# Kernel tuning notes

Hardware: AMD Instinct MI355X
Metric: run time of the kernel (lower is better)

## Reference

```python
import jax, jax.numpy as jnp
import numpy as np

B, N, D, DEPTH = 1, 512, 128, 4


def mlp_apply(W, x):
    # W: (depth, d, d), x: (..., d). First layer has no activation, then silu before each matmul.
    x = x @ W[0]
    for i in range(1, DEPTH):
        x = jax.nn.silu(x) @ W[i]
    return x


def _binop(x, y):
    # linear recurrence combine: s_t = a_t * s_{t-1} + b_t
    a1, b1 = x
    a2, b2 = y
    return (a1 * a2, a2 * b1 + b2)


def setup_inputs() -> dict:
    key = jax.random.key(0)
    ks = jax.random.split(key, 7)
    s = 0.02  # scale for projection weights (torch Linear-like init magnitude)
    return {
        "seq": jax.random.normal(ks[0], (B, N, D), jnp.float32),
        "W_mem": jax.random.normal(ks[1], (DEPTH, D, D), jnp.float32) * (D ** -0.5),
        "W_q": jax.random.normal(ks[2], (D, D), jnp.float32) * s,
        "W_kv": jax.random.normal(ks[3], (D, 2 * D), jnp.float32) * s,
        "W_mom": jax.random.normal(ks[4], (D, 1), jnp.float32) * s,
        "W_step": jax.random.normal(ks[5], (D, 1), jnp.float32) * s,
        "W_decay": jax.random.normal(ks[6], (D, 1), jnp.float32) * s,
    }


def reference(seq, W_mem, W_q, W_kv, W_mom, W_step, W_decay):
    b, n, d = seq.shape
    # --- store_memories ---
    adaptive_lr = (seq @ W_step)[..., 0]            # (b, n)
    adaptive_mom = seq @ W_mom                      # (b, n, 1)
    decay = jax.nn.sigmoid(seq @ W_decay)           # (b, n, 1)

    kv = seq.reshape(b * n, d) @ W_kv               # (bn, 2d)
    keys, values = kv[:, :d], kv[:, d:]

    def loss_fn(W, k, v):
        pred = mlp_apply(W, k)                      # (d,)
        # (pred - v)^2 .mean(-1).sum() for a single sample == mean over d
        return jnp.mean((pred - v) ** 2)

    # per-sample meta-gradients wrt memory MLP weights
    losses, grads = jax.vmap(jax.value_and_grad(loss_fn, argnums=0), in_axes=(None, 0, 0))(W_mem, keys, values)
    grads = grads.reshape(b, n, DEPTH, d, d)
    surprise = grads * (-adaptive_lr)[..., None, None, None]   # (b,n,depth,d,d)

    # momentum_t = adaptive_mom_t * momentum_{t-1} + surprise_t  (assoc. scan over n)
    am = adaptive_mom[..., None, None]              # (b, n, 1, 1, 1)
    _, momentum = jax.lax.associative_scan(_binop, (am, surprise), axis=1)

    # update_t = (1 - decay_t) * update_{t-1} + momentum_t
    dec = (1.0 - decay)[..., None, None]            # (b, n, 1, 1, 1)
    _, updates = jax.lax.associative_scan(_binop, (dec, momentum), axis=1)

    # --- retrieve_memories with per-token updated weights ---
    q = (seq @ W_q).reshape(b * n, d)
    W_tok = (W_mem[None, None] + updates).reshape(b * n, DEPTH, d, d)
    retrieved = jax.vmap(mlp_apply)(W_tok, q).reshape(b, n, d)
    return retrieved
```

## Files before the change

kernel.cpp:

```cpp
#include <hip/hip_runtime.h>
#include <hip/hip_bf16.h>
#include <math.h>

#define N 512
#define D 128
#define DD (D*D)
#define ND (N*D)
#define LSTR 132
#define CSTR 36

__device__ __forceinline__ float sigmoidf_(float x) { return 1.f / (1.f + expf(-x)); }

__global__ void k_transpose(const float* __restrict__ W_mem, float* __restrict__ WT) {
    int idx = blockIdx.x * 256 + threadIdx.x;
    int l = idx / DD;
    int r = idx % DD;
    int i = r / D;
    int j = r % D;
    WT[idx] = W_mem[(l + 1) * DD + j * D + i];
}

__global__ __launch_bounds__(512) void k_phase1(
    const float* __restrict__ seq, const float* __restrict__ W_mem,
    const float* __restrict__ W_q, const float* __restrict__ W_kv,
    const float* __restrict__ W_mom, const float* __restrict__ W_step,
    const float* __restrict__ W_decay, const float* __restrict__ WT,
    float* __restrict__ Q, float* __restrict__ INS, float* __restrict__ ES,
    float* __restrict__ am, float* __restrict__ dec)
{
    __shared__ float s_seq[D], s_v[D], s_cur[D];
    __shared__ float s_h[4][D];
    __shared__ float s_part[4][D];
    __shared__ float s_p3[4][3][D];
    __shared__ float s_red[8];
    __shared__ float s_lr;

    const int t = blockIdx.x;
    const int tid = threadIdx.x;
    const int j = tid & 127;
    const int p = tid >> 7;
    const int i0 = p * 32;

    if (p == 0) s_seq[j] = seq[t * D + j];
    __syncthreads();

    float ps = 0.f;
    if (p == 1) ps = s_seq[j] * W_step[j];
    else if (p == 2) ps = s_seq[j] * W_mom[j];
    else if (p == 3) ps = s_seq[j] * W_decay[j];
#pragma unroll
    for (int off = 32; off > 0; off >>= 1) ps += __shfl_down(ps, off);
    if ((tid & 63) == 0) s_red[tid >> 6] = ps;
    __syncthreads();
    if (tid == 0) s_lr = s_red[2] + s_red[3];
    else if (tid == 1) am[t] = s_red[4] + s_red[5];
    else if (tid == 2) dec[t] = 1.f - sigmoidf_(s_red[6] + s_red[7]);

    float kp = 0.f, vp = 0.f, qp = 0.f;
#pragma unroll 8
    for (int ii = 0; ii < 32; ii++) {
        int i = i0 + ii;
        float si = s_seq[i];
        kp += si * W_kv[i * 256 + j];
        vp += si * W_kv[i * 256 + 128 + j];
        qp += si * W_q[i * 128 + j];
    }
    s_p3[p][0][j] = kp; s_p3[p][1][j] = vp; s_p3[p][2][j] = qp;
    __syncthreads();
    if (p == 0) {
        float kj = s_p3[0][0][j] + s_p3[1][0][j] + s_p3[2][0][j] + s_p3[3][0][j];
        s_cur[j] = kj;
        INS[t * D + j] = kj;
    } else if (p == 1) {
        s_v[j] = s_p3[0][1][j] + s_p3[1][1][j] + s_p3[2][1][j] + s_p3[3][1][j];
    } else if (p == 2) {
        Q[t * D + j] = s_p3[0][2][j] + s_p3[1][2][j] + s_p3[2][2][j] + s_p3[3][2][j];
    }
    __syncthreads();

    for (int l = 0; l < 4; l++) {
        const float* Wl = W_mem + l * DD;
        float yp = 0.f;
#pragma unroll 8
        for (int ii = 0; ii < 32; ii++) {
            int i = i0 + ii;
            yp += s_cur[i] * Wl[i * D + j];
        }
        s_part[p][j] = yp;
        __syncthreads();
        if (p == 0) {
            float y = s_part[0][j] + s_part[1][j] + s_part[2][j] + s_part[3][j];
            s_h[l][j] = y;
            if (l < 3) {
                float a = y * sigmoidf_(y);
                s_cur[j] = a;
                INS[(l + 1) * ND + t * D + j] = a;
            }
        }
        __syncthreads();
    }

    if (p == 0) {
        float e = -s_lr * (2.f / (float)D) * (s_h[3][j] - s_v[j]);
        ES[3 * ND + t * D + j] = e;
        s_cur[j] = e;
    }
    __syncthreads();

    for (int l = 3; l >= 1; l--) {
        const float* Wt = WT + (l - 1) * DD;
        float gp = 0.f;
#pragma unroll 8
        for (int ii = 0; ii < 32; ii++) {
            int i = i0 + ii;
            gp += s_cur[i] * Wt[i * D + j];
        }
        s_part[p][j] = gp;
        __syncthreads();
        if (p == 0) {
            float g = s_part[0][j] + s_part[1][j] + s_part[2][j] + s_part[3][j];
            float h = s_h[l - 1][j];
            float sg = sigmoidf_(h);
            float e2 = g * (sg * (1.f + h * (1.f - sg)));
            ES[(l - 1) * ND + t * D + j] = e2;
            s_cur[j] = e2;
        }
        __syncthreads();
    }
}

__global__ __launch_bounds__(512) void k_logscan(
    const float* __restrict__ am, const float* __restrict__ dec,
    double* __restrict__ LA, double* __restrict__ LDp, int* __restrict__ NC)
{
    __shared__ double sa[N], sd[N];
    __shared__ int sn[N];
    const int t = threadIdx.x;
    float a = am[t];
    float d = dec[t];
    sa[t] = log((double)fmaxf(fabsf(a), 1e-38f));
    sd[t] = log((double)fmaxf(d, 1e-38f));
    sn[t] = (a < 0.f) ? 1 : 0;
    __syncthreads();
    for (int off = 1; off < N; off <<= 1) {
        double va = 0.0, vd = 0.0; int vn = 0;
        if (t >= off) { va = sa[t - off]; vd = sd[t - off]; vn = sn[t - off]; }
        __syncthreads();
        sa[t] += va; sd[t] += vd; sn[t] += vn;
        __syncthreads();
    }
    LA[t] = sa[t]; LDp[t] = sd[t]; NC[t] = sn[t];
}

__global__ __launch_bounds__(256) void k_build(
    const double* __restrict__ LA, const double* __restrict__ LDp,
    const int* __restrict__ NC,
    float* __restrict__ Amat, float* __restrict__ Dmat)
{
    int idx = blockIdx.x * 256 + threadIdx.x;
    int u = idx >> 9;
    int s = idx & (N - 1);
    float va = 0.f, vd = 0.f;
    if (s <= u) {
        va = expf((float)(LA[u] - LA[s]));
        if ((NC[u] - NC[s]) & 1) va = -va;
        vd = expf((float)(LDp[u] - LDp[s]));
    }
    Amat[idx] = va;
    Dmat[idx] = vd;
}

__global__ __launch_bounds__(256) void k_betamm(
    const float* __restrict__ Dmat, const float* __restrict__ Amat,
    float* __restrict__ beta)
{
    const int bs = blockIdx.x;
    const int bt = blockIdx.y;
    const int tx = threadIdx.x & 31;
    const int ty = threadIdx.x >> 5;

    if (bs > bt) {
#pragma unroll
        for (int j = 0; j < 4; j++)
            beta[(bt * 32 + ty + 8 * j) * N + bs * 32 + tx] = 0.f;
        return;
    }

    __shared__ float sD[32][33];
    __shared__ float sA[32][33];
    float acc[4] = {0.f, 0.f, 0.f, 0.f};

    for (int kt = bs; kt <= bt; kt++) {
        for (int i = threadIdx.x; i < 1024; i += 256) {
            int r = i >> 5, c = i & 31;
            sD[r][c] = Dmat[(bt * 32 + r) * N + kt * 32 + c];
            sA[r][c] = Amat[(kt * 32 + r) * N + bs * 32 + c];
        }
        __syncthreads();
#pragma unroll 8
        for (int k = 0; k < 32; k++) {
            float a = sA[k][tx];
#pragma unroll
            for (int j = 0; j < 4; j++)
                acc[j] += sD[ty + 8 * j][k] * a;
        }
        __syncthreads();
    }
#pragma unroll
    for (int j = 0; j < 4; j++)
        beta[(bt * 32 + ty + 8 * j) * N + bs * 32 + tx] = acc[j];
}

__global__ __launch_bounds__(256) void k_layer(
    const float* __restrict__ Xsrc, float* __restrict__ Pout,
    const float* __restrict__ Wl, const float* __restrict__ INSl,
    const float* __restrict__ ESl, const float* __restrict__ beta,
    int mode)
{
    const int r = blockIdx.x;
    const int z = blockIdx.y;
    const bool isW = (z == 8);
    if (!isW && 4 * z > r) return;
    const int t0 = r * 16;
    const int lane = threadIdx.x;

    __shared__ float sX[16 * LSTR];
    __shared__ float sI[32 * LSTR];
    __shared__ float sE[32 * LSTR];
    __shared__ float sc[16 * CSTR];

    const int nzs = (r >> 2) + 1;
#pragma unroll
    for (int i = 0; i < 2; i++) {
        int f4 = lane + 256 * i;
        int row = f4 >> 5, c4 = f4 & 31;
        float4 v = ((const float4*)(Xsrc + t0 * D))[f4];
        if (mode) {
            for (int zz = 1; zz < nzs; zz++) {
                float4 u = ((const float4*)(Xsrc + zz * ND + t0 * D))[f4];
                v.x += u.x; v.y += u.y; v.z += u.z; v.w += u.w;
            }
            float4 w = ((const float4*)(Xsrc + 8 * ND + t0 * D))[f4];
            v.x += w.x; v.y += w.y; v.z += w.z; v.w += w.w;
            v.x = v.x * sigmoidf_(v.x); v.y = v.y * sigmoidf_(v.y);
            v.z = v.z * sigmoidf_(v.z); v.w = v.w * sigmoidf_(v.w);
        }
        *(float4*)(sX + row * LSTR + c4 * 4) = v;
    }

    const int ti  = lane >> 4;
    const int q15 = lane & 15;
    const int j8  = q15 * 8;

    if (isW) {
        __syncthreads();
        float acc[8];
#pragma unroll
        for (int b = 0; b < 8; b++) acc[b] = 0.f;
#pragma unroll 4
        for (int k = 0; k < D; k++) {
            float4 w0 = *(const float4*)(Wl + k * D + j8);
            float4 w1 = *(const float4*)(Wl + k * D + j8 + 4);
            float xv = sX[ti * LSTR + k];
            acc[0] += xv * w0.x; acc[1] += xv * w0.y;
            acc[2] += xv * w0.z; acc[3] += xv * w0.w;
            acc[4] += xv * w1.x; acc[5] += xv * w1.y;
            acc[6] += xv * w1.z; acc[7] += xv * w1.w;
        }
        float* yp = Pout + 8 * ND + (t0 + ti) * D + j8;
        *(float4*)yp       = make_float4(acc[0], acc[1], acc[2], acc[3]);
        *(float4*)(yp + 4) = make_float4(acc[4], acc[5], acc[6], acc[7]);
        return;
    }

    const int si0 = q15 * 2;
    float acc[8];
#pragma unroll
    for (int b = 0; b < 8; b++) acc[b] = 0.f;

    for (int sub = 0; sub < 2; sub++) {
        const int s0 = z * 64 + sub * 32;
        __syncthreads();
#pragma unroll
        for (int i = 0; i < 4; i++) {
            int f4 = lane + 256 * i;
            int row = f4 >> 5, c4 = f4 & 31;
            float4 a = ((const float4*)(INSl + s0 * D))[f4];
            float4 b = ((const float4*)(ESl + s0 * D))[f4];
            *(float4*)(sI + row * LSTR + c4 * 4) = a;
            *(float4*)(sE + row * LSTR + c4 * 4) = b;
        }
        float b0 = beta[(t0 + ti) * N + s0 + si0];
        float b1 = beta[(t0 + ti) * N + s0 + si0 + 1];
        __syncthreads();

        float g0 = 0.f, g1 = 0.f;
#pragma unroll 8
        for (int k4 = 0; k4 < D; k4 += 4) {
            float4 a  = *(float4*)(sX + ti * LSTR + k4);
            float4 p0 = *(float4*)(sI + si0 * LSTR + k4);
            float4 p1 = *(float4*)(sI + (si0 + 1) * LSTR + k4);
            g0 += a.x * p0.x + a.y * p0.y + a.z * p0.z + a.w * p0.w;
            g1 += a.x * p1.x + a.y * p1.y + a.z * p1.z + a.w * p1.w;
        }
        sc[ti * CSTR + si0]     = g0 * b0;
        sc[ti * CSTR + si0 + 1] = g1 * b1;
        __syncthreads();

#pragma unroll 8
        for (int s = 0; s < 32; s++) {
            float cv = sc[ti * CSTR + s];
            float4 e0 = *(float4*)(sE + s * LSTR + j8);
            float4 e1 = *(float4*)(sE + s * LSTR + j8 + 4);
            acc[0] += cv * e0.x; acc[1] += cv * e0.y;
            acc[2] += cv * e0.z; acc[3] += cv * e0.w;
            acc[4] += cv * e1.x; acc[5] += cv * e1.y;
            acc[6] += cv * e1.z; acc[7] += cv * e1.w;
        }
    }

    float* yp = Pout + z * ND + (t0 + ti) * D + j8;
    *(float4*)yp       = make_float4(acc[0], acc[1], acc[2], acc[3]);
    *(float4*)(yp + 4) = make_float4(acc[4], acc[5], acc[6], acc[7]);
}

__global__ __launch_bounds__(256) void k_reduce(
    const float* __restrict__ P, float* __restrict__ out)
{
    int f4 = blockIdx.x * 256 + threadIdx.x;
    int t = f4 >> 5;
    int r = t >> 4;
    int nzs = (r >> 2) + 1;
    float4 v = ((const float4*)P)[f4];
    for (int zz = 1; zz < nzs; zz++) {
        float4 u = ((const float4*)(P + zz * ND))[f4];
        v.x += u.x; v.y += u.y; v.z += u.z; v.w += u.w;
    }
    float4 w = ((const float4*)(P + 8 * ND))[f4];
    v.x += w.x; v.y += w.y; v.z += w.z; v.w += w.w;
    ((float4*)out)[f4] = v;
}

extern "C" void kernel_launch(void* const* d_in, const int* in_sizes, int n_in,
                              void* d_out, int out_size, void* d_ws, size_t ws_size,
                              hipStream_t stream) {
    const float* seq     = (const float*)d_in[0];
    const float* W_mem   = (const float*)d_in[1];
    const float* W_q     = (const float*)d_in[2];
    const float* W_kv    = (const float*)d_in[3];
    const float* W_mom   = (const float*)d_in[4];
    const float* W_step  = (const float*)d_in[5];
    const float* W_decay = (const float*)d_in[6];
    float* out = (float*)d_out;

    float* ws   = (float*)d_ws;
    float* am   = ws;
    float* dec  = am + N;
    float* Q    = dec + N;
    float* INS  = Q + ND;
    float* ES   = INS + 4 * ND;
    float* beta = ES + 4 * ND;
    float* WT   = beta + N * N;
    float* Amat = WT + 3 * DD;
    float* Dmat = Amat + N * N;
    float* Pa   = Dmat + N * N;
    float* Pb   = Pa + 9 * ND;
    double* LA  = (double*)(Pb + 9 * ND);
    double* LDp = LA + N;
    int* NC     = (int*)(LDp + N);

    k_transpose<<<192, 256, 0, stream>>>(W_mem, WT);
    k_phase1<<<N, 512, 0, stream>>>(seq, W_mem, W_q, W_kv, W_mom, W_step, W_decay,
                                    WT, Q, INS, ES, am, dec);
    k_logscan<<<1, N, 0, stream>>>(am, dec, LA, LDp, NC);
    k_build<<<(N * N) / 256, 256, 0, stream>>>(LA, LDp, NC, Amat, Dmat);
    dim3 mmgrid(N / 32, N / 32);
    k_betamm<<<mmgrid, 256, 0, stream>>>(Dmat, Amat, beta);

    dim3 lgrid(32, 9);
    k_layer<<<lgrid, 256, 0, stream>>>(Q,  Pa, W_mem,          INS,          ES,          beta, 0);
    k_layer<<<lgrid, 256, 0, stream>>>(Pa, Pb, W_mem + DD,     INS + ND,     ES + ND,     beta, 1);
    k_layer<<<lgrid, 256, 0, stream>>>(Pb, Pa, W_mem + 2 * DD, INS + 2 * ND, ES + 2 * ND, beta, 1);
    k_layer<<<lgrid, 256, 0, stream>>>(Pa, Pb, W_mem + 3 * DD, INS + 3 * ND, ES + 3 * ND, beta, 1);
    k_reduce<<<64, 256, 0, stream>>>(Pb, out);
}
```

Measured before the change: 202.2 us.

## Split beta matmul along K into partial tiles and add reduction kernel

The triangular beta matmul now splits each output tile's K range into up to four chunks across a third grid dimension, writing partial sums into a scratch buffer (reusing Pa), and a new kernel sums those partials. The inner loop also switches to a 2x2 register tile with float2 shared-memory loads from a transposed D tile. The aim is to spread the long diagonal-distant tiles across more blocks so the matmul is less limited by its slowest tiles, at the cost of an extra launch and extra global traffic for the partials.

```diff
diff --git a/kernel.cpp b/kernel.cpp
--- a/kernel.cpp
+++ b/kernel.cpp
@@ -3,6 +3,7 @@
 #include <math.h>
 
 #define N 512
+#define NN (N*N)
 #define D 128
 #define DD (D*D)
 #define ND (N*D)
@@ -172,43 +173,66 @@
 
 __global__ __launch_bounds__(256) void k_betamm(
     const float* __restrict__ Dmat, const float* __restrict__ Amat,
-    float* __restrict__ beta)
+    float* __restrict__ betaP)
 {
     const int bs = blockIdx.x;
     const int bt = blockIdx.y;
-    const int tx = threadIdx.x & 31;
-    const int ty = threadIdx.x >> 5;
-
-    if (bs > bt) {
-#pragma unroll
-        for (int j = 0; j < 4; j++)
-            beta[(bt * 32 + ty + 8 * j) * N + bs * 32 + tx] = 0.f;
-        return;
-    }
-
-    __shared__ float sD[32][33];
-    __shared__ float sA[32][33];
-    float acc[4] = {0.f, 0.f, 0.f, 0.f};
-
-    for (int kt = bs; kt <= bt; kt++) {
-        for (int i = threadIdx.x; i < 1024; i += 256) {
+    const int z  = blockIdx.z;
+    if (bs > bt) return;
+    const int span = bt - bs + 1;
+    const int chunk = (span + 3) >> 2;
+    const int kBeg = bs + z * chunk;
+    const int kEnd = (kBeg + chunk < bt + 1) ? (kBeg + chunk) : (bt + 1);
+    if (kBeg >= kEnd) return;
+
+    __shared__ float sA[32 * 34];
+    __shared__ float sDT[32 * 34];
+
+    const int tid = threadIdx.x;
+    const int tx = tid & 15;
+    const int ty = tid >> 4;
+    float acc00 = 0.f, acc01 = 0.f, acc10 = 0.f, acc11 = 0.f;
+
+    for (int kt = kBeg; kt < kEnd; kt++) {
+        for (int i = tid; i < 1024; i += 256) {
             int r = i >> 5, c = i & 31;
-            sD[r][c] = Dmat[(bt * 32 + r) * N + kt * 32 + c];
-            sA[r][c] = Amat[(kt * 32 + r) * N + bs * 32 + c];
+            sA[r * 34 + c]  = Amat[(kt * 32 + r) * N + bs * 32 + c];
+            sDT[c * 34 + r] = Dmat[(bt * 32 + r) * N + kt * 32 + c];
         }
         __syncthreads();
 #pragma unroll 8
         for (int k = 0; k < 32; k++) {
-            float a = sA[k][tx];
-#pragma unroll
-            for (int j = 0; j < 4; j++)
-                acc[j] += sD[ty + 8 * j][k] * a;
-        }
-        __syncthreads();
-    }
-#pragma unroll
-    for (int j = 0; j < 4; j++)
-        beta[(bt * 32 + ty + 8 * j) * N + bs * 32 + tx] = acc[j];
+            float2 a = *(float2*)&sA[k * 34 + 2 * tx];
+            float2 d = *(float2*)&sDT[k * 34 + 2 * ty];
+            acc00 += d.x * a.x; acc01 += d.x * a.y;
+            acc10 += d.y * a.x; acc11 += d.y * a.y;
+        }
+        __syncthreads();
+    }
+    float* bp = betaP + z * NN + (bt * 32 + 2 * ty) * N + bs * 32 + 2 * tx;
+    *(float2*)bp       = make_float2(acc00, acc01);
+    *(float2*)(bp + N) = make_float2(acc10, acc11);
+}
+
+__global__ __launch_bounds__(256) void k_betared(
+    const float* __restrict__ betaP, float* __restrict__ beta)
+{
+    int idx4 = blockIdx.x * 256 + threadIdx.x;
+    int t  = idx4 >> 7;
+    int s0 = (idx4 & 127) * 4;
+    int bt = t >> 5, bs = s0 >> 5;
+    float4 v = make_float4(0.f, 0.f, 0.f, 0.f);
+    if (bs <= bt) {
+        int span = bt - bs + 1;
+        int chunk = (span + 3) >> 2;
+        int nz = (span + chunk - 1) / chunk;
+        v = *(const float4*)(betaP + t * N + s0);
+        for (int z = 1; z < nz; z++) {
+            float4 u = *(const float4*)(betaP + z * NN + t * N + s0);
+            v.x += u.x; v.y += u.y; v.z += u.z; v.w += u.w;
+        }
+    }
+    *(float4*)(beta + t * N + s0) = v;
 }
 
 __global__ __launch_bounds__(256) void k_layer(
@@ -360,22 +384,24 @@
     float* INS  = Q + ND;
     float* ES   = INS + 4 * ND;
     float* beta = ES + 4 * ND;
-    float* WT   = beta + N * N;
+    float* WT   = beta + NN;
     float* Amat = WT + 3 * DD;
-    float* Dmat = Amat + N * N;
-    float* Pa   = Dmat + N * N;
+    float* Dmat = Amat + NN;
+    float* Pa   = Dmat + NN;
     float* Pb   = Pa + 9 * ND;
     double* LA  = (double*)(Pb + 9 * ND);
     double* LDp = LA + N;
     int* NC     = (int*)(LDp + N);
+    float* betaP = Pa;
 
     k_transpose<<<192, 256, 0, stream>>>(W_mem, WT);
     k_phase1<<<N, 512, 0, stream>>>(seq, W_mem, W_q, W_kv, W_mom, W_step, W_decay,
                                     WT, Q, INS, ES, am, dec);
     k_logscan<<<1, N, 0, stream>>>(am, dec, LA, LDp, NC);
-    k_build<<<(N * N) / 256, 256, 0, stream>>>(LA, LDp, NC, Amat, Dmat);
-    dim3 mmgrid(N / 32, N / 32);
-    k_betamm<<<mmgrid, 256, 0, stream>>>(Dmat, Amat, beta);
+    k_build<<<(NN) / 256, 256, 0, stream>>>(LA, LDp, NC, Amat, Dmat);
+    dim3 mmgrid(N / 32, N / 32, 4);
+    k_betamm<<<mmgrid, 256, 0, stream>>>(Dmat, Amat, betaP);
+    k_betared<<<NN / 4 / 256, 256, 0, stream>>>(betaP, beta);
 
     dim3 lgrid(32, 9);
     k_layer<<<lgrid, 256, 0, stream>>>(Q,  Pa, W_mem,          INS,          ES,          beta, 0);
```

Result: faster. 173.5 us (-14.2%).
